# Kernel optimization log

Measured on AMD Instinct MI355X. Metric: run time of the kernel, lower is better.

Reference implementation:

```python
import jax, jax.numpy as jnp
import numpy as np

B, L, D, VOCAB, LAYERS = 4, 1024, 512, 32000, 4


def setup_inputs() -> dict:
    key = jax.random.key(0)
    ks = jax.random.split(key, 6)
    s = 0.02
    return {
        "input_ids": jax.random.randint(ks[0], (B, L), 0, VOCAB, dtype=jnp.int32),
        "embed": jax.random.normal(ks[1], (VOCAB, D), dtype=jnp.float32) * s,
        "starter": jax.random.normal(ks[2], (LAYERS, D), dtype=jnp.float32) * s,
        "W": jax.random.normal(ks[3], (LAYERS, 2 * D, 2 * D), dtype=jnp.float32) * s,
        "b": jnp.zeros((LAYERS, 2 * D), dtype=jnp.float32),
        "Wout": jax.random.normal(ks[4], (VOCAB, D), dtype=jnp.float32) * s,
        "bout": jnp.zeros((VOCAB,), dtype=jnp.float32),
    }


def reference(input_ids, embed, starter, W, b, Wout, bout):
    Bsz, Lsz = input_ids.shape
    d = starter.shape[-1]
    x = embed[input_ids]                      # [B, L, D]
    xT = jnp.transpose(x, (1, 0, 2))          # [L, B, D] time-major for scan
    s0 = jnp.broadcast_to(starter[:, None, :], (LAYERS, Bsz, d))  # [layers, B, D]

    def layer_step(x_cur, inp):
        Wi, bi, si = inp                      # Wi [2D,2D] (torch out-in), bi [2D], si [B,D]
        xs = jnp.concatenate([x_cur, si], axis=-1) @ Wi.T + bi    # [B, 2D]
        x_new, s_new = jnp.split(xs, 2, axis=-1)
        return x_new, s_new

    def time_step(s_stack, x_t):
        y, new_s = jax.lax.scan(layer_step, x_t, (W, b, s_stack))
        return new_s, y

    _, ys = jax.lax.scan(time_step, s0, xT)   # ys [L, B, D]
    logits = jnp.einsum('lbd,vd->blv', ys, Wout) + bout           # [B, L, V]
    return logits
```

## Files before the change

### kernel.cpp

```cpp
#include <hip/hip_runtime.h>

typedef unsigned short u16;
typedef unsigned int u32;
typedef __attribute__((ext_vector_type(8))) short bf16x8;
typedef __attribute__((ext_vector_type(4))) float f32x4;
typedef __attribute__((ext_vector_type(8))) u16 u16x8;

__device__ __forceinline__ u16 f2b(float f) {
  u32 u = __builtin_bit_cast(u32, f);
  u += 0x7fffu + ((u >> 16) & 1u);
  return (u16)(u >> 16);
}
__device__ __forceinline__ float b2f(u16 h) {
  u32 u = ((u32)h) << 16;
  return __builtin_bit_cast(float, u);
}
__device__ __forceinline__ f32x4 mfma16(bf16x8 a, bf16x8 b, f32x4 c) {
  return __builtin_amdgcn_mfma_f32_16x16x32_bf16(a, b, c, 0, 0, 0);
}

__global__ __launch_bounds__(256) void cast_w_kernel(const float* __restrict__ W,
                                                     u16* __restrict__ Wb,
                                                     u16* __restrict__ WbT) {
  __shared__ u16 tile[64][65];
  int L = blockIdx.z, R0 = blockIdx.y * 64, C0 = blockIdx.x * 64;
  const float* Wl = W + (size_t)L * (1024 * 1024);
  u16* Wbl = Wb + (size_t)L * (1024 * 1024);
  u16* WbTl = WbT + (size_t)L * (1024 * 1024);
  int tr = threadIdx.x >> 6, tc = threadIdx.x & 63;
  for (int i = 0; i < 16; ++i) {
    int r = tr * 16 + i;
    u16 v = f2b(Wl[(size_t)(R0 + r) * 1024 + C0 + tc]);
    Wbl[(size_t)(R0 + r) * 1024 + C0 + tc] = v;
    tile[r][tc] = v;
  }
  __syncthreads();
  for (int i = 0; i < 16; ++i) {
    int r = tr * 16 + i;
    WbTl[(size_t)(C0 + r) * 1024 + R0 + tc] = tile[tc][r];
  }
}

__global__ __launch_bounds__(256) void cast_f32_bf16_kernel(const float* __restrict__ in,
                                                            u16* __restrict__ out, long n8) {
  long i = (long)blockIdx.x * 256 + threadIdx.x;
  long stride = (long)gridDim.x * 256;
  for (; i < n8; i += stride) {
    const float* s = in + i * 8;
    u16x8 o;
#pragma unroll
    for (int j = 0; j < 8; ++j) o[j] = f2b(s[j]);
    *(u16x8*)(out + i * 8) = o;
  }
}

__global__ __launch_bounds__(256) void gather_e_kernel(const int* __restrict__ ids,
                                                       const float* __restrict__ embed,
                                                       u16* __restrict__ ebf) {
  int row = blockIdx.x * 4 + (threadIdx.x >> 6);
  int lane = threadIdx.x & 63;
  int t = row >> 2, b = row & 3;
  int id = ids[b * 1024 + t];
  const float* src = embed + (size_t)id * 512 + lane * 8;
  u16x8 o;
#pragma unroll
  for (int j = 0; j < 8; ++j) o[j] = f2b(src[j]);
  *(u16x8*)(ebf + (size_t)row * 512 + lane * 8) = o;
}

__global__ __launch_bounds__(256) void init_s0_kernel(const float* __restrict__ starter,
                                                      u16* __restrict__ Sall) {
  int i = blockIdx.x * 256 + threadIdx.x;
  if (i < 2048) {
    u16 v = f2b(starter[i]);
    for (int b = 0; b < 4; ++b) Sall[(size_t)b * 2048 + i] = v;
  }
}

__global__ __launch_bounds__(256) void assemble_kernel(const u16* __restrict__ Wb,
                                                       const u16* __restrict__ WbT,
                                                       u16* __restrict__ M, u16* __restrict__ MT,
                                                       u16* __restrict__ Rm, u16* __restrict__ Um) {
  int task = blockIdx.y;
  int e = blockIdx.x * 256 + threadIdx.x;
  int r = e >> 9, c = e & 511;
  if (task < 4) {
    int i = task;
    u16 v = Wb[(size_t)i * 1048576 + (size_t)(512 + r) * 1024 + 512 + c];
    u16 vt = WbT[(size_t)i * 1048576 + (size_t)(512 + r) * 1024 + 512 + c];
    M[(size_t)(i * 512 + r) * 2048 + i * 512 + c] = v;
    MT[(size_t)(i * 512 + r) * 2048 + i * 512 + c] = vt;
  } else if (task == 4) {
    Rm[(size_t)r * 2048 + 3 * 512 + c] = Wb[(size_t)3 * 1048576 + (size_t)r * 1024 + 512 + c];
  } else {
    Um[(size_t)r * 512 + c] = Wb[(size_t)(512 + r) * 1024 + c];
  }
}

__global__ __launch_bounds__(256) void bias_step_kernel(const float* __restrict__ W,
                                                        const float* __restrict__ bv, int layer,
                                                        const float* __restrict__ hin,
                                                        float* __restrict__ hout,
                                                        float* __restrict__ kvec) {
  int wid = threadIdx.x >> 6, lane = threadIdx.x & 63;
  int gw = blockIdx.x * 4 + wid;
  for (int o = gw; o < 1024; o += 64) {
    const float* row = W + (size_t)layer * 1048576 + (size_t)o * 1024;
    float s = 0.f;
    for (int k = lane; k < 512; k += 64) s += row[k] * hin[k];
    for (int off = 32; off; off >>= 1) s += __shfl_down(s, off);
    if (lane == 0) {
      float v = s + bv[layer * 1024 + o];
      if (o < 512) hout[o] = v;
      else kvec[layer * 512 + (o - 512)] = v;
    }
  }
}

struct G512 { const u16* A; const u16* B; u16* C; u16* CT; int lda, ldb, ldc, ldt; };
struct G512Args { G512 g[8]; };

__global__ __launch_bounds__(256) void gemm512_kernel(G512Args args) {
  G512 d = args.g[blockIdx.z];
  int wid = threadIdx.x >> 6, lane = threadIdx.x & 63;
  int wr = wid >> 1, wc = wid & 1;
  int row0 = blockIdx.y * 64 + wr * 32, col0 = blockIdx.x * 64 + wc * 32;
  int fr = lane & 15, fk = (lane >> 4) * 8;
  f32x4 acc[2][2] = {};
  for (int kk = 0; kk < 512; kk += 32) {
    bf16x8 a[2], b[2];
#pragma unroll
    for (int m = 0; m < 2; ++m)
      a[m] = *(const bf16x8*)(d.A + (size_t)(row0 + m * 16 + fr) * d.lda + kk + fk);
#pragma unroll
    for (int n = 0; n < 2; ++n)
      b[n] = *(const bf16x8*)(d.B + (size_t)(col0 + n * 16 + fr) * d.ldb + kk + fk);
#pragma unroll
    for (int m = 0; m < 2; ++m)
#pragma unroll
      for (int n = 0; n < 2; ++n) acc[m][n] = mfma16(a[m], b[n], acc[m][n]);
  }
  int dr = (lane >> 4) * 4, dc = lane & 15;
  for (int m = 0; m < 2; ++m)
    for (int n = 0; n < 2; ++n)
#pragma unroll
      for (int j = 0; j < 4; ++j) {
        int r = row0 + m * 16 + dr + j, c = col0 + n * 16 + dc;
        u16 v = f2b(acc[m][n][j]);
        d.C[(size_t)r * d.ldc + c] = v;
        if (d.CT) d.CT[(size_t)c * d.ldt + r] = v;
      }
}

template <bool OUT_BF16, bool WRITE_T, bool PERM, bool ADD_PREV, bool HAS_BIAS>
__global__ __launch_bounds__(256) void gemm128_kernel(
    const u16* __restrict__ A, int lda, const u16* __restrict__ B, int ldb, int K,
    void* __restrict__ C, int ldc, u16* __restrict__ CT, int ldt,
    const float* __restrict__ bias, const float* __restrict__ prev, int ldp) {
  __shared__ u16 As[128 * 64];
  __shared__ u16 Bs[128 * 64];
  int tid = threadIdx.x;
  int wid = tid >> 6, lane = tid & 63;
  int wr = wid >> 1, wc = wid & 1;
  int fr = lane & 15, fkb = (lane >> 4) * 8;
  int rowt = blockIdx.y * 128, colt = blockIdx.x * 128;
  f32x4 acc[4][4] = {};
  for (int kk = 0; kk < K; kk += 64) {
#pragma unroll
    for (int i = 0; i < 4; ++i) {
      int q = i * 256 + tid;
      int r = q >> 3, kc = (q & 7) * 8;
      *(bf16x8*)&As[r * 64 + kc] = *(const bf16x8*)(A + (size_t)(rowt + r) * lda + kk + kc);
      *(bf16x8*)&Bs[r * 64 + kc] = *(const bf16x8*)(B + (size_t)(colt + r) * ldb + kk + kc);
    }
    __syncthreads();
#pragma unroll
    for (int kh = 0; kh < 64; kh += 32) {
      bf16x8 a[4], b[4];
#pragma unroll
      for (int m = 0; m < 4; ++m) a[m] = *(const bf16x8*)&As[(wr * 64 + m * 16 + fr) * 64 + kh + fkb];
#pragma unroll
      for (int n = 0; n < 4; ++n) b[n] = *(const bf16x8*)&Bs[(wc * 64 + n * 16 + fr) * 64 + kh + fkb];
#pragma unroll
      for (int m = 0; m < 4; ++m)
#pragma unroll
        for (int n = 0; n < 4; ++n) acc[m][n] = mfma16(a[m], b[n], acc[m][n]);
    }
    __syncthreads();
  }
  int dr = (lane >> 4) * 4, dc = lane & 15;
  for (int m = 0; m < 4; ++m)
    for (int n = 0; n < 4; ++n) {
      int c = colt + wc * 64 + n * 16 + dc;
      float bvv = HAS_BIAS ? bias[c] : 0.f;
#pragma unroll
      for (int j = 0; j < 4; ++j) {
        int r = rowt + wr * 64 + m * 16 + dr + j;
        float v = acc[m][n][j] + bvv;
        if (ADD_PREV) v += prev[(size_t)r * ldp + c];
        int orow = PERM ? ((r & 3) * 1024 + (r >> 2)) : r;
        if (OUT_BF16) ((u16*)C)[(size_t)orow * ldc + c] = f2b(v);
        else ((float*)C)[(size_t)orow * ldc + c] = v;
        if (WRITE_T) CT[(size_t)c * ldt + r] = f2b(v);
      }
    }
}

__global__ __launch_bounds__(256) void scan_step_kernel(
    const u16* __restrict__ Abase, size_t acs, const u16* __restrict__ M,
    const u16* __restrict__ Vbase, size_t vcs, u16* __restrict__ Obase, size_t ocs, int nch) {
  __shared__ float red[4 * 32 * 32];
  int tid = threadIdx.x, wid = tid >> 6, lane = tid & 63;
  int rt = blockIdx.y * 32, ct = blockIdx.x * 32;
  int fr = lane & 15, fk = (lane >> 4) * 8;
  int kw = wid * 512;
  f32x4 acc[2][2] = {};
  const u16* arow[2];
#pragma unroll
  for (int m = 0; m < 2; ++m) {
    int r = rt + m * 16 + fr;
    int cc = r >> 2;
    if (cc >= nch) cc = nch - 1;
    arow[m] = Abase + (size_t)cc * acs + (size_t)(r & 3) * 2048;
  }
  for (int kk = 0; kk < 512; kk += 32) {
    int k = kw + kk + fk;
    bf16x8 a[2], b[2];
#pragma unroll
    for (int m = 0; m < 2; ++m) a[m] = *(const bf16x8*)(arow[m] + k);
#pragma unroll
    for (int n = 0; n < 2; ++n) b[n] = *(const bf16x8*)(M + (size_t)(ct + n * 16 + fr) * 2048 + k);
#pragma unroll
    for (int m = 0; m < 2; ++m)
#pragma unroll
      for (int n = 0; n < 2; ++n) acc[m][n] = mfma16(a[m], b[n], acc[m][n]);
  }
  int dr = (lane >> 4) * 4, dc = lane & 15;
#pragma unroll
  for (int m = 0; m < 2; ++m)
#pragma unroll
    for (int n = 0; n < 2; ++n)
#pragma unroll
      for (int j = 0; j < 4; ++j)
        red[wid * 1024 + (m * 16 + dr + j) * 32 + n * 16 + dc] = acc[m][n][j];
  __syncthreads();
  for (int t = 0; t < 4; ++t) {
    int o = t * 256 + tid;
    int rl = o >> 5, cl = o & 31;
    int r = rt + rl;
    int cc = r >> 2;
    if (cc < nch) {
      float s = red[rl * 32 + cl] + red[1024 + rl * 32 + cl] + red[2048 + rl * 32 + cl] +
                red[3072 + rl * 32 + cl];
      s += b2f(Vbase[(size_t)cc * vcs + (size_t)(r & 3) * 2048 + ct + cl]);
      Obase[(size_t)cc * ocs + (size_t)(r & 3) * 2048 + ct + cl] = f2b(s);
    }
  }
}

__global__ __launch_bounds__(256) void copy_v0_kernel(const u16* __restrict__ vbuf,
                                                      u16* __restrict__ ping) {
  int r = blockIdx.x;
  int c = r >> 2, b = r & 3;
  const uint4* src = (const uint4*)(vbuf + (size_t)c * 262144 + (size_t)b * 2048);
  uint4* dst = (uint4*)(ping + (size_t)r * 2048);
  dst[threadIdx.x] = src[threadIdx.x];
}

static inline size_t alignup(size_t x) { return (x + 255) & ~(size_t)255; }

extern "C" void kernel_launch(void* const* d_in, const int* in_sizes, int n_in,
                              void* d_out, int out_size, void* d_ws, size_t ws_size,
                              hipStream_t stream) {
  const int* ids = (const int*)d_in[0];
  const float* embed = (const float*)d_in[1];
  const float* starter = (const float*)d_in[2];
  const float* W = (const float*)d_in[3];
  const float* bvec = (const float*)d_in[4];
  const float* Wout = (const float*)d_in[5];
  const float* bout = (const float*)d_in[6];
  float* out = (float*)d_out;

  char* p = (char*)d_ws;
  auto alloc = [&](size_t bytes) { char* q = p; p += alignup(bytes); return q; };
  u16* Wbf = (u16*)alloc(8388608);
  u16* WbT = (u16*)alloc(8388608);
  u16* Mm = (u16*)alloc(8388608);
  u16* MTm = (u16*)alloc(8388608);
  u16* SQ0 = (u16*)alloc(8388608);
  u16* SQ1 = (u16*)alloc(8388608);
  u16* SQ2 = (u16*)alloc(8388608);
  u16* SQ3 = (u16*)alloc(8388608);
  u16* X2 = (u16*)alloc(524288);  u16* X2T = (u16*)alloc(524288);
  u16* X3 = (u16*)alloc(524288);  u16* X3T = (u16*)alloc(524288);
  u16* P1 = (u16*)alloc(524288);  u16* P1T = (u16*)alloc(524288);
  u16* P2 = (u16*)alloc(524288);  u16* P2T = (u16*)alloc(524288);
  u16* P3 = (u16*)alloc(524288);  u16* P3T = (u16*)alloc(524288);
  u16* Um = (u16*)alloc(2097152);
  u16* Rm = (u16*)alloc(2097152);
  u16* Qm = (u16*)alloc(524288);
  u16* ebf = (u16*)alloc(4194304);
  u16* vbuf = (u16*)alloc(16777216);
  u16* Sall = (u16*)alloc(16777216);
  u16* ping0 = (u16*)alloc(524288);
  u16* ping1 = (u16*)alloc(524288);
  float* yacc = (float*)alloc(8388608);
  u16* ybf = (u16*)alloc(4194304);
  u16* WoutB = (u16*)alloc(32768000);
  float* kvec = (float*)alloc(8192);
  float* h0 = (float*)alloc(2048);
  float* h1 = (float*)alloc(2048);
  if ((size_t)(p - (char*)d_ws) > ws_size) return;

  hipMemsetAsync(Mm, 0, 16777216, stream);
  hipMemsetAsync(h0, 0, 2048, stream);

  cast_w_kernel<<<dim3(16, 16, 4), 256, 0, stream>>>(W, Wbf, WbT);
  cast_f32_bf16_kernel<<<4096, 256, 0, stream>>>(Wout, WoutB, 32000L * 512 / 8);
  gather_e_kernel<<<1024, 256, 0, stream>>>(ids, embed, ebf);
  init_s0_kernel<<<8, 256, 0, stream>>>(starter, Sall);
  assemble_kernel<<<dim3(1024, 6), 256, 0, stream>>>(Wbf, WbT, Mm, MTm, Rm, Um);

  {
    const float* hin = h0;
    float* hout = h1;
    for (int l = 0; l < 4; ++l) {
      bias_step_kernel<<<16, 256, 0, stream>>>(W, bvec, l, hin, hout, kvec);
      float* t = (float*)hin; hin = hout; hout = t;
    }
  }
  const float* cvec = h0;

  auto wb = [&](int i) { return Wbf + (size_t)i * 1048576; };
  auto wbt = [&](int i) { return WbT + (size_t)i * 1048576; };
  const size_t Apos = 0, Cpos = (size_t)512 * 1024;
  auto mblk = [&](int i, int j) { return Mm + (size_t)(i * 512) * 2048 + j * 512; };
  auto mtblk = [&](int i, int j) { return MTm + (size_t)(j * 512) * 2048 + i * 512; };

  {
    G512Args a{};
    int n = 0;
    auto add = [&](const u16* A_, int lda, const u16* B_, int ldb, u16* C_, int ldc, u16* CT_, int ldt) {
      a.g[n++] = G512{A_, B_, C_, CT_, lda, ldb, ldc, ldt};
    };
    add(wb(1) + Apos, 1024, wbt(0) + Apos, 1024, X2, 512, X2T, 512);
    add(wb(1) + Apos, 1024, wbt(0) + Cpos, 1024, P1, 512, P1T, 512);
    add(wb(2) + Apos, 1024, wbt(1) + Cpos, 1024, P3, 512, P3T, 512);
    add(wb(1) + Cpos, 1024, wbt(0) + Cpos, 1024, mblk(1, 0), 2048, mtblk(1, 0), 2048);
    add(wb(2) + Cpos, 1024, wbt(1) + Cpos, 1024, mblk(2, 1), 2048, mtblk(2, 1), 2048);
    add(wb(3) + Apos, 1024, wbt(2) + Cpos, 1024, Rm + 2 * 512, 2048, nullptr, 0);
    add(wb(3) + Cpos, 1024, wbt(2) + Cpos, 1024, mblk(3, 2), 2048, mtblk(3, 2), 2048);
    add(wb(1) + Cpos, 1024, wbt(0) + Apos, 1024, Um + (size_t)1 * 262144, 512, nullptr, 0);
    gemm512_kernel<<<dim3(8, 8, 8), 256, 0, stream>>>(a);
  }
  {
    G512Args a{};
    int n = 0;
    auto add = [&](const u16* A_, int lda, const u16* B_, int ldb, u16* C_, int ldc, u16* CT_, int ldt) {
      a.g[n++] = G512{A_, B_, C_, CT_, lda, ldb, ldc, ldt};
    };
    add(wb(2) + Apos, 1024, X2T, 512, X3, 512, X3T, 512);
    add(wb(2) + Apos, 1024, P1T, 512, P2, 512, P2T, 512);
    add(wb(2) + Cpos, 1024, P1T, 512, mblk(2, 0), 2048, mtblk(2, 0), 2048);
    add(wb(3) + Apos, 1024, P3T, 512, Rm + 512, 2048, nullptr, 0);
    add(wb(3) + Cpos, 1024, P3T, 512, mblk(3, 1), 2048, mtblk(3, 1), 2048);
    add(wb(2) + Cpos, 1024, X2T, 512, Um + (size_t)2 * 262144, 512, nullptr, 0);
    gemm512_kernel<<<dim3(8, 8, 6), 256, 0, stream>>>(a);
  }
  {
    G512Args a{};
    int n = 0;
    auto add = [&](const u16* A_, int lda, const u16* B_, int ldb, u16* C_, int ldc, u16* CT_, int ldt) {
      a.g[n++] = G512{A_, B_, C_, CT_, lda, ldb, ldc, ldt};
    };
    add(wb(3) + Apos, 1024, X3T, 512, Qm, 512, nullptr, 0);
    add(wb(3) + Apos, 1024, P2T, 512, Rm, 2048, nullptr, 0);
    add(wb(3) + Cpos, 1024, P2T, 512, mblk(3, 0), 2048, mtblk(3, 0), 2048);
    add(wb(3) + Cpos, 1024, X3T, 512, Um + (size_t)3 * 262144, 512, nullptr, 0);
    gemm512_kernel<<<dim3(8, 8, 4), 256, 0, stream>>>(a);
  }

  u16* cur = Mm;
  u16* curT = MTm;
  for (int s = 0; s < 5; ++s) {
    u16* nx = (s & 1) ? SQ2 : SQ0;
    u16* nxT = (s & 1) ? SQ3 : SQ1;
    gemm128_kernel<true, true, false, false, false><<<dim3(16, 16), 256, 0, stream>>>(
        cur, 2048, curT, 2048, 2048, (void*)nx, 2048, nxT, 2048, nullptr, nullptr, 0);
    cur = nx; curT = nxT;
  }
  u16* M32 = cur;

  gemm128_kernel<true, false, false, false, true><<<dim3(16, 32), 256, 0, stream>>>(
      ebf, 512, Um, 512, 512, (void*)vbuf, 2048, nullptr, 0, kvec, nullptr, 0);

  copy_v0_kernel<<<128, 256, 0, stream>>>(vbuf, ping0);
  u16* pg[2] = {ping0, ping1};
  int pc = 0;
  for (int j = 1; j < 32; ++j) {
    scan_step_kernel<<<dim3(64, 4), 256, 0, stream>>>(
        pg[pc], 8192, Mm, vbuf + (size_t)j * 8192, 262144, pg[pc ^ 1], 8192, 32);
    pc ^= 1;
  }
  u16* wstack = pg[pc];

  for (int c = 0; c < 31; ++c) {
    scan_step_kernel<<<dim3(64, 1), 256, 0, stream>>>(
        Sall + (size_t)c * 262144, 0, M32, wstack + (size_t)c * 8192, 0,
        Sall + (size_t)(c + 1) * 262144, 0, 1);
  }

  for (int j = 0; j < 31; ++j) {
    scan_step_kernel<<<dim3(64, 4), 256, 0, stream>>>(
        Sall + (size_t)j * 8192, 262144, Mm, vbuf + (size_t)j * 8192, 262144,
        Sall + (size_t)(j + 1) * 8192, 262144, 32);
  }

  gemm128_kernel<false, false, false, false, false><<<dim3(4, 32), 256, 0, stream>>>(
      Sall, 2048, Rm, 2048, 2048, (void*)yacc, 512, nullptr, 0, nullptr, nullptr, 0);
  gemm128_kernel<true, false, false, true, true><<<dim3(4, 32), 256, 0, stream>>>(
      ebf, 512, Qm, 512, 512, (void*)ybf, 512, nullptr, 0, cvec, yacc, 512);

  gemm128_kernel<false, false, true, false, true><<<dim3(250, 32), 256, 0, stream>>>(
      ybf, 512, WoutB, 512, 512, (void*)out, 32000, nullptr, 0, bout, nullptr, 0);
}
```

Measured before the change: 1.792 ms.

## Fuse scan steps into one cooperative kernel and exploit block-triangular structure

The roughly 93 separate scan_step launches are replaced by a single cooperative kernel that uses grid.sync between steps. Each step's K range is limited to the nonzero lower-triangular part of the block matrix. The five matrix-squaring GEMMs now run only the 10 nonzero lower-triangular 512-blocks with a reduced K. The output GEMM gains a block-index swizzle for L2 reuse, and the M memset is removed. The aim is to cut launch overhead and skip work on zero blocks, at the cost of relying on grid-wide barriers, cooperative-launch residency, and zero blocks never being read.

Result: slower. 4.031 ms (+124.9%).

```diff
diff --git a/kernel.cpp b/kernel.cpp
--- a/kernel.cpp
+++ b/kernel.cpp
@@ -1,4 +1,5 @@
 #include <hip/hip_runtime.h>
+#include <hip/hip_cooperative_groups.h>
 
 typedef unsigned short u16;
 typedef unsigned int u32;
@@ -152,10 +153,65 @@
       }
 }
 
-template <bool OUT_BF16, bool WRITE_T, bool PERM, bool ADD_PREV, bool HAS_BIAS>
+__global__ __launch_bounds__(256) void sq_tri_kernel(const u16* __restrict__ Mc,
+                                                     const u16* __restrict__ McT,
+                                                     u16* __restrict__ Mo,
+                                                     u16* __restrict__ MoT) {
+  __shared__ u16 As[128 * 64];
+  __shared__ u16 Bs[128 * 64];
+  const int ti_[10] = {0, 1, 1, 2, 2, 2, 3, 3, 3, 3};
+  const int tj_[10] = {0, 0, 1, 0, 1, 2, 0, 1, 2, 3};
+  int t = blockIdx.z;
+  int ib = ti_[t], jb = tj_[t];
+  int K = (ib - jb + 1) << 9;
+  const u16* A = Mc + (size_t)(ib * 512) * 2048 + jb * 512;
+  const u16* B = McT + (size_t)(jb * 512) * 2048 + jb * 512;
+  int tid = threadIdx.x;
+  int wid = tid >> 6, lane = tid & 63;
+  int wr = wid >> 1, wc = wid & 1;
+  int fr = lane & 15, fkb = (lane >> 4) * 8;
+  int rowt = blockIdx.y * 128, colt = blockIdx.x * 128;
+  f32x4 acc[4][4] = {};
+  for (int kk = 0; kk < K; kk += 64) {
+#pragma unroll
+    for (int i = 0; i < 4; ++i) {
+      int q = i * 256 + tid;
+      int r = q >> 3, kc = (q & 7) * 8;
+      *(bf16x8*)&As[r * 64 + kc] = *(const bf16x8*)(A + (size_t)(rowt + r) * 2048 + kk + kc);
+      *(bf16x8*)&Bs[r * 64 + kc] = *(const bf16x8*)(B + (size_t)(colt + r) * 2048 + kk + kc);
+    }
+    __syncthreads();
+#pragma unroll
+    for (int kh = 0; kh < 64; kh += 32) {
+      bf16x8 a[4], b[4];
+#pragma unroll
+      for (int m = 0; m < 4; ++m) a[m] = *(const bf16x8*)&As[(wr * 64 + m * 16 + fr) * 64 + kh + fkb];
+#pragma unroll
+      for (int n = 0; n < 4; ++n) b[n] = *(const bf16x8*)&Bs[(wc * 64 + n * 16 + fr) * 64 + kh + fkb];
+#pragma unroll
+      for (int m = 0; m < 4; ++m)
+#pragma unroll
+        for (int n = 0; n < 4; ++n) acc[m][n] = mfma16(a[m], b[n], acc[m][n]);
+    }
+    __syncthreads();
+  }
+  int dr = (lane >> 4) * 4, dc = lane & 15;
+  for (int m = 0; m < 4; ++m)
+    for (int n = 0; n < 4; ++n)
+#pragma unroll
+      for (int j = 0; j < 4; ++j) {
+        int r = rowt + wr * 64 + m * 16 + dr + j;
+        int c = colt + wc * 64 + n * 16 + dc;
+        u16 v = f2b(acc[m][n][j]);
+        Mo[(size_t)(ib * 512 + r) * 2048 + jb * 512 + c] = v;
+        MoT[(size_t)(jb * 512 + c) * 2048 + ib * 512 + r] = v;
+      }
+}
+
+template <bool OUT_BF16, bool PERM, bool ADD_PREV, bool HAS_BIAS, bool SWZ>
 __global__ __launch_bounds__(256) void gemm128_kernel(
     const u16* __restrict__ A, int lda, const u16* __restrict__ B, int ldb, int K,
-    void* __restrict__ C, int ldc, u16* __restrict__ CT, int ldt,
+    void* __restrict__ C, int ldc,
     const float* __restrict__ bias, const float* __restrict__ prev, int ldp) {
   __shared__ u16 As[128 * 64];
   __shared__ u16 Bs[128 * 64];
@@ -163,7 +219,16 @@
   int wid = tid >> 6, lane = tid & 63;
   int wr = wid >> 1, wc = wid & 1;
   int fr = lane & 15, fkb = (lane >> 4) * 8;
-  int rowt = blockIdx.y * 128, colt = blockIdx.x * 128;
+  int rowt, colt;
+  if (SWZ) {
+    int bid = blockIdx.x;
+    int lin = (bid & 7) * 1000 + (bid >> 3);
+    rowt = (lin & 31) * 128;
+    colt = (lin >> 5) * 128;
+  } else {
+    rowt = blockIdx.y * 128;
+    colt = blockIdx.x * 128;
+  }
   f32x4 acc[4][4] = {};
   for (int kk = 0; kk < K; kk += 64) {
 #pragma unroll
@@ -201,70 +266,99 @@
         int orow = PERM ? ((r & 3) * 1024 + (r >> 2)) : r;
         if (OUT_BF16) ((u16*)C)[(size_t)orow * ldc + c] = f2b(v);
         else ((float*)C)[(size_t)orow * ldc + c] = v;
-        if (WRITE_T) CT[(size_t)c * ldt + r] = f2b(v);
       }
     }
 }
 
-__global__ __launch_bounds__(256) void scan_step_kernel(
-    const u16* __restrict__ Abase, size_t acs, const u16* __restrict__ M,
-    const u16* __restrict__ Vbase, size_t vcs, u16* __restrict__ Obase, size_t ocs, int nch) {
-  __shared__ float red[4 * 32 * 32];
-  int tid = threadIdx.x, wid = tid >> 6, lane = tid & 63;
-  int rt = blockIdx.y * 32, ct = blockIdx.x * 32;
+__device__ __forceinline__ void step128(const u16* __restrict__ Abase, int a_cs,
+                                        const u16* __restrict__ M,
+                                        const u16* __restrict__ Vbase, int v_cs,
+                                        u16* __restrict__ Obase, int o_cs,
+                                        int ct, int rg, int wv, int lane) {
+  int i_blk = ct >> 3;
+  int Keff = (i_blk + 1) << 9;
   int fr = lane & 15, fk = (lane >> 4) * 8;
-  int kw = wid * 512;
-  f32x4 acc[2][2] = {};
-  const u16* arow[2];
-#pragma unroll
-  for (int m = 0; m < 2; ++m) {
-    int r = rt + m * 16 + fr;
-    int cc = r >> 2;
-    if (cc >= nch) cc = nch - 1;
-    arow[m] = Abase + (size_t)cc * acs + (size_t)(r & 3) * 2048;
-  }
-  for (int kk = 0; kk < 512; kk += 32) {
-    int k = kw + kk + fk;
-    bf16x8 a[2], b[2];
-#pragma unroll
-    for (int m = 0; m < 2; ++m) a[m] = *(const bf16x8*)(arow[m] + k);
-#pragma unroll
-    for (int n = 0; n < 2; ++n) b[n] = *(const bf16x8*)(M + (size_t)(ct + n * 16 + fr) * 2048 + k);
-#pragma unroll
-    for (int m = 0; m < 2; ++m)
-#pragma unroll
-      for (int n = 0; n < 2; ++n) acc[m][n] = mfma16(a[m], b[n], acc[m][n]);
+  int r0 = rg * 64 + wv * 16;
+  int ar = r0 + fr;
+  const u16* Arow = Abase + (size_t)(ar >> 2) * a_cs + (size_t)(ar & 3) * 2048;
+  const u16* Mbase = M + (size_t)(ct * 64 + fr) * 2048;
+  f32x4 acc[4] = {};
+  for (int k = 0; k < Keff; k += 32) {
+    bf16x8 a = *(const bf16x8*)(Arow + k + fk);
+#pragma unroll
+    for (int n = 0; n < 4; ++n) {
+      bf16x8 b = *(const bf16x8*)(Mbase + (size_t)n * 32768 + k + fk);
+      acc[n] = mfma16(a, b, acc[n]);
+    }
   }
   int dr = (lane >> 4) * 4, dc = lane & 15;
 #pragma unroll
-  for (int m = 0; m < 2; ++m)
-#pragma unroll
-    for (int n = 0; n < 2; ++n)
-#pragma unroll
-      for (int j = 0; j < 4; ++j)
-        red[wid * 1024 + (m * 16 + dr + j) * 32 + n * 16 + dc] = acc[m][n][j];
-  __syncthreads();
-  for (int t = 0; t < 4; ++t) {
-    int o = t * 256 + tid;
-    int rl = o >> 5, cl = o & 31;
-    int r = rt + rl;
-    int cc = r >> 2;
-    if (cc < nch) {
-      float s = red[rl * 32 + cl] + red[1024 + rl * 32 + cl] + red[2048 + rl * 32 + cl] +
-                red[3072 + rl * 32 + cl];
-      s += b2f(Vbase[(size_t)cc * vcs + (size_t)(r & 3) * 2048 + ct + cl]);
-      Obase[(size_t)cc * ocs + (size_t)(r & 3) * 2048 + ct + cl] = f2b(s);
-    }
-  }
-}
-
-__global__ __launch_bounds__(256) void copy_v0_kernel(const u16* __restrict__ vbuf,
-                                                      u16* __restrict__ ping) {
-  int r = blockIdx.x;
-  int c = r >> 2, b = r & 3;
-  const uint4* src = (const uint4*)(vbuf + (size_t)c * 262144 + (size_t)b * 2048);
-  uint4* dst = (uint4*)(ping + (size_t)r * 2048);
-  dst[threadIdx.x] = src[threadIdx.x];
+  for (int n = 0; n < 4; ++n) {
+    int col = ct * 64 + n * 16 + dc;
+#pragma unroll
+    for (int j = 0; j < 4; ++j) {
+      int rr = r0 + dr + j;
+      size_t voff = (size_t)(rr >> 2) * v_cs + (size_t)(rr & 3) * 2048 + col;
+      size_t ooff = (size_t)(rr >> 2) * o_cs + (size_t)(rr & 3) * 2048 + col;
+      Obase[ooff] = f2b(acc[n][j] + b2f(Vbase[voff]));
+    }
+  }
+}
+
+__device__ __forceinline__ void step4(const u16* __restrict__ A, const u16* __restrict__ M32,
+                                      const u16* __restrict__ V, u16* __restrict__ O,
+                                      int ct, int wv, int lane) {
+  int i_blk = ct >> 3;
+  int Keff = (i_blk + 1) << 9;
+  int fr = lane & 15, fk = (lane >> 4) * 8;
+  int ar = fr < 4 ? fr : 3;
+  const u16* Arow = A + (size_t)ar * 2048;
+  const u16* Mb = M32 + (size_t)(ct * 64 + wv * 16 + fr) * 2048;
+  f32x4 acc = {};
+  for (int k = 0; k < Keff; k += 32) {
+    bf16x8 a = *(const bf16x8*)(Arow + k + fk);
+    bf16x8 b = *(const bf16x8*)(Mb + k + fk);
+    acc = mfma16(a, b, acc);
+  }
+  int dr = (lane >> 4) * 4, dc = lane & 15;
+  int col = ct * 64 + wv * 16 + dc;
+#pragma unroll
+  for (int j = 0; j < 4; ++j) {
+    int rr = dr + j;
+    if (rr < 4) O[(size_t)rr * 2048 + col] = f2b(acc[j] + b2f(V[(size_t)rr * 2048 + col]));
+  }
+}
+
+__global__ __launch_bounds__(256) void scan_coop_kernel(
+    const u16* __restrict__ M, const u16* __restrict__ M32, const u16* __restrict__ vbuf,
+    u16* __restrict__ Sall, u16* __restrict__ ping0, u16* __restrict__ ping1) {
+  cooperative_groups::grid_group grid = cooperative_groups::this_grid();
+  int blk = blockIdx.x;
+  int ct = blk >> 1, rg = blk & 1;
+  int wv = threadIdx.x >> 6, lane = threadIdx.x & 63;
+
+  const u16* A = vbuf;
+  int a_cs = 262144;
+  for (int j = 1; j <= 31; ++j) {
+    u16* O = (j & 1) ? ping0 : ping1;
+    step128(A, a_cs, M, vbuf + (size_t)j * 8192, 262144, O, 8192, ct, rg, wv, lane);
+    grid.sync();
+    A = O;
+    a_cs = 8192;
+  }
+
+  for (int c = 0; c < 31; ++c) {
+    if (rg == 0)
+      step4(Sall + (size_t)c * 262144, M32, ping0 + (size_t)c * 8192,
+            Sall + (size_t)(c + 1) * 262144, ct, wv, lane);
+    grid.sync();
+  }
+
+  for (int j = 0; j < 31; ++j) {
+    step128(Sall + (size_t)j * 8192, 262144, M, vbuf + (size_t)j * 8192, 262144,
+            Sall + (size_t)(j + 1) * 8192, 262144, ct, rg, wv, lane);
+    grid.sync();
+  }
 }
 
 static inline size_t alignup(size_t x) { return (x + 255) & ~(size_t)255; }
@@ -312,7 +406,6 @@
   float* h1 = (float*)alloc(2048);
   if ((size_t)(p - (char*)d_ws) > ws_size) return;
 
-  hipMemsetAsync(Mm, 0, 16777216, stream);
   hipMemsetAsync(h0, 0, 2048, stream);
 
   cast_w_kernel<<<dim3(16, 16, 4), 256, 0, stream>>>(W, Wbf, WbT);
@@ -385,42 +478,25 @@
   for (int s = 0; s < 5; ++s) {
     u16* nx = (s & 1) ? SQ2 : SQ0;
     u16* nxT = (s & 1) ? SQ3 : SQ1;
-    gemm128_kernel<true, true, false, false, false><<<dim3(16, 16), 256, 0, stream>>>(
-        cur, 2048, curT, 2048, 2048, (void*)nx, 2048, nxT, 2048, nullptr, nullptr, 0);
+    sq_tri_kernel<<<dim3(4, 4, 10), 256, 0, stream>>>(cur, curT, nx, nxT);
     cur = nx; curT = nxT;
   }
   u16* M32 = cur;
 
-  gemm128_kernel<true, false, false, false, true><<<dim3(16, 32), 256, 0, stream>>>(
-      ebf, 512, Um, 512, 512, (void*)vbuf, 2048, nullptr, 0, kvec, nullptr, 0);
-
-  copy_v0_kernel<<<128, 256, 0, stream>>>(vbuf, ping0);
-  u16* pg[2] = {ping0, ping1};
-  int pc = 0;
-  for (int j = 1; j < 32; ++j) {
-    scan_step_kernel<<<dim3(64, 4), 256, 0, stream>>>(
-        pg[pc], 8192, Mm, vbuf + (size_t)j * 8192, 262144, pg[pc ^ 1], 8192, 32);
-    pc ^= 1;
-  }
-  u16* wstack = pg[pc];
-
-  for (int c = 0; c < 31; ++c) {
-    scan_step_kernel<<<dim3(64, 1), 256, 0, stream>>>(
-        Sall + (size_t)c * 262144, 0, M32, wstack + (size_t)c * 8192, 0,
-        Sall + (size_t)(c + 1) * 262144, 0, 1);
-  }
-
-  for (int j = 0; j < 31; ++j) {
-    scan_step_kernel<<<dim3(64, 4), 256, 0, stream>>>(
-        Sall + (size_t)j * 8192, 262144, Mm, vbuf + (size_t)j * 8192, 262144,
-        Sall + (size_t)(j + 1) * 8192, 262144, 32);
+  gemm128_kernel<true, false, false, true, false><<<dim3(16, 32), 256, 0, stream>>>(
+      ebf, 512, Um, 512, 512, (void*)vbuf, 2048, kvec, nullptr, 0);
+
+  {
+    void* args[] = {(void*)&Mm, (void*)&M32, (void*)&vbuf, (void*)&Sall,
+                    (void*)&ping0, (void*)&ping1};
+    hipLaunchCooperativeKernel((void*)scan_coop_kernel, dim3(64), dim3(256), args, 0, stream);
   }
 
   gemm128_kernel<false, false, false, false, false><<<dim3(4, 32), 256, 0, stream>>>(
-      Sall, 2048, Rm, 2048, 2048, (void*)yacc, 512, nullptr, 0, nullptr, nullptr, 0);
-  gemm128_kernel<true, false, false, true, true><<<dim3(4, 32), 256, 0, stream>>>(
-      ebf, 512, Qm, 512, 512, (void*)ybf, 512, nullptr, 0, cvec, yacc, 512);
-
-  gemm128_kernel<false, false, true, false, true><<<dim3(250, 32), 256, 0, stream>>>(
-      ybf, 512, WoutB, 512, 512, (void*)out, 32000, nullptr, 0, bout, nullptr, 0);
-}
+      Sall, 2048, Rm, 2048, 2048, (void*)yacc, 512, nullptr, nullptr, 0);
+  gemm128_kernel<true, false, true, true, false><<<dim3(4, 32), 256, 0, stream>>>(
+      ebf, 512, Qm, 512, 512, (void*)ybf, 512, cvec, yacc, 512);
+
+  gemm128_kernel<false, true, false, true, true><<<dim3(8000), 256, 0, stream>>>(
+      ybf, 512, WoutB, 512, 512, (void*)out, 32000, bout, nullptr, 0);
+}
```
